# Optimization experiments

Hardware: AMD Instinct MI355X
Metric: run time of the kernel (lower is better)

## Reference

```python
import jax, jax.numpy as jnp
import numpy as np

NUM_NODES = 20000
NUM_EDGES = 65536
WIDTH = 64
EDGE_FEAT = 6
HIDDEN = 128


def setup_inputs() -> dict:
    key = jax.random.key(0)
    ks = jax.random.split(key, 6)
    x = jax.random.normal(ks[0], (NUM_NODES, WIDTH), dtype=jnp.float32)
    edge_attr = jax.random.normal(ks[1], (NUM_EDGES, EDGE_FEAT), dtype=jnp.float32)
    # weight-generating MLP params (the `nn` callable), fan-in scaled
    W1 = jax.random.normal(ks[2], (EDGE_FEAT, HIDDEN), dtype=jnp.float32) / np.sqrt(EDGE_FEAT)
    b1 = jnp.zeros((HIDDEN,), dtype=jnp.float32)
    W2 = jax.random.normal(ks[3], (HIDDEN, WIDTH * WIDTH), dtype=jnp.float32) / np.sqrt(HIDDEN)
    b2 = jnp.zeros((WIDTH * WIDTH,), dtype=jnp.float32)
    senders = jax.random.randint(ks[4], (NUM_EDGES,), 0, NUM_NODES)
    receivers = jax.random.randint(ks[5], (NUM_EDGES,), 0, NUM_NODES)
    return {"x": x, "edge_attr": edge_attr, "W1": W1, "b1": b1,
            "W2": W2, "b2": b2, "senders": senders, "receivers": receivers}


def reference(x, edge_attr, W1, b1, W2, b2, senders, receivers):
    n_segs, width = x.shape
    # nn(edge_attr): (E, width*width) edge-conditioned weights
    h = jax.nn.relu(edge_attr @ W1 + b1)
    weight = (h @ W2 + b2).reshape(-1, width, width)  # (E, w, w)
    # gather sender features, per-edge (1,w) @ (w,w) matmul -> (E, w)
    msgs = jnp.einsum('ew,ewv->ev', x[senders], weight)
    # scatter-sum messages into receiver nodes (aggr == 'sum')
    return jax.ops.segment_sum(msgs, receivers, num_segments=n_segs)
```

## Files before the change

### kernel.cpp

```cpp
#include <hip/hip_runtime.h>
#include <stdint.h>

typedef _Float16 f16;
typedef f16 f16x8 __attribute__((ext_vector_type(8)));
typedef float f32x4 __attribute__((ext_vector_type(4)));

#define NUM_NODES 20000
#define NUM_EDGES 65536
#define WIDTH 64
#define EDGE_FEAT 6
#define HIDDEN 128
#define BM 128
#define PADCH 132
#define XPAD 72

#define XH_HALFS (NUM_NODES * WIDTH)
#define XCONV_BLKS 625
#define W2G_HALFS (PADCH * 4096)
#define OUT_FLOATS (NUM_NODES * WIDTH)
#define ZBLKS 313

__device__ __forceinline__ void gload_lds16(const f16* g, f16* l) {
  __builtin_amdgcn_global_load_lds(
      (const __attribute__((address_space(1))) unsigned int*)g,
      (__attribute__((address_space(3))) unsigned int*)l, 16, 0, 0);
}

__global__ __launch_bounds__(256) void prep_kernel(
    const float* __restrict__ x, const float* __restrict__ W2,
    const float* __restrict__ b2, f16* __restrict__ ws_h,
    float* __restrict__ out)
{
  f16* x_h = ws_h;
  f16* W2g = ws_h + XH_HALFS;
  const int blk = blockIdx.x, tid = threadIdx.x;

  if (blk < PADCH) {
    const int ki = blk;
    if (ki > HIDDEN) {
      f16x8 z;
      #pragma unroll
      for (int u = 0; u < 8; ++u) z[u] = (f16)0.f;
      *(f16x8*)&W2g[(size_t)ki * 4096 + tid * 16] = z;
      *(f16x8*)&W2g[(size_t)ki * 4096 + tid * 16 + 8] = z;
      return;
    }
    __shared__ float row[4096];
    const float* srcrow;
    if (ki < HIDDEN) {
      const float4* src = (const float4*)(W2 + (size_t)ki * 4096);
      #pragma unroll
      for (int i = 0; i < 4; ++i) {
        float4 v = src[tid + 256 * i];
        *(float4*)&row[(tid + 256 * i) * 4] = v;
      }
      __syncthreads();
      srcrow = row;
    } else {
      srcrow = b2;
    }
    const int obase = tid * 16;
    f16x8 outv0, outv1;
    #pragma unroll
    for (int u = 0; u < 8; ++u) {
      int o = obase + u;
      int n = o >> 6, pg = (o >> 3) & 7, j = o & 7;
      int k = (pg ^ (n & 7)) * 8 + j;
      outv0[u] = (f16)srcrow[k * 64 + n];
    }
    #pragma unroll
    for (int u = 0; u < 8; ++u) {
      int o = obase + 8 + u;
      int n = o >> 6, pg = (o >> 3) & 7, j = o & 7;
      int k = (pg ^ (n & 7)) * 8 + j;
      outv1[u] = (f16)srcrow[k * 64 + n];
    }
    *(f16x8*)&W2g[(size_t)ki * 4096 + obase] = outv0;
    *(f16x8*)&W2g[(size_t)ki * 4096 + obase + 8] = outv1;
  } else if (blk < PADCH + XCONV_BLKS) {
    int idx = (blk - PADCH) * 2048 + tid * 8;
    if (idx + 8 <= XH_HALFS) {
      float4 a = *(const float4*)(x + idx);
      float4 b = *(const float4*)(x + idx + 4);
      f16x8 hv;
      hv[0] = (f16)a.x; hv[1] = (f16)a.y; hv[2] = (f16)a.z; hv[3] = (f16)a.w;
      hv[4] = (f16)b.x; hv[5] = (f16)b.y; hv[6] = (f16)b.z; hv[7] = (f16)b.w;
      *(f16x8*)&x_h[idx] = hv;
    }
  } else {
    int base = (blk - PADCH - XCONV_BLKS) * 4096 + tid * 16;
    float4 z = {0.f, 0.f, 0.f, 0.f};
    #pragma unroll
    for (int i = 0; i < 4; ++i) {
      int idx = base + i * 4;
      if (idx + 4 <= OUT_FLOATS) *(float4*)(out + idx) = z;
    }
  }
}

__global__ __launch_bounds__(256, 3) void nnconv_kernel(
    const float* __restrict__ ea, const float* __restrict__ W1,
    const float* __restrict__ b1, const int* __restrict__ senders,
    const int* __restrict__ receivers, const f16* __restrict__ ws_h,
    float* __restrict__ out)
{
  const f16* x_h = ws_h;
  const f16* W2g = ws_h + XH_HALFS;
  __shared__ __align__(16) f16 xt[BM][XPAD];
  __shared__ __align__(16) f16 Bring[2 * 8192];

  const int tid = threadIdx.x;
  const int lane = tid & 63, wid = tid >> 6;
  const int quad = lane >> 4, l15 = lane & 15;
  const int mhalf = wid >> 1, nhalf = wid & 1;
  const int e0 = blockIdx.x * BM;
  const int mbase = mhalf * 64;

#define STAGE(GIDX, GP)                                                       \
  {                                                                           \
    _Pragma("unroll") for (int i_ = 0; i_ < 4; ++i_) {                        \
      int slice_ = wid + 4 * i_;                                              \
      gload_lds16(W2g + (size_t)(GIDX) * 8192 + slice_ * 512 + (lane << 3),   \
                  &Bring[(GP) * 8192 + slice_ * 512]);                        \
    }                                                                         \
  }
  STAGE(0, 0);

  {
    int r = tid >> 1, half = tid & 1;
    int s = senders[e0 + r];
    const uint4* src = (const uint4*)(x_h + (size_t)s * WIDTH + half * 32);
    uint4* dst = (uint4*)&xt[r][half * 32];
    #pragma unroll
    for (int i = 0; i < 4; ++i) dst[i] = src[i];
  }

  float ear[4][6];
  #pragma unroll
  for (int t = 0; t < 4; ++t) {
    const float* p = ea + (size_t)(e0 + mbase + t * 16 + l15) * EDGE_FEAT;
    #pragma unroll
    for (int f = 0; f < 6; ++f) ear[t][f] = p[f];
  }

  int boff[2][2];
  #pragma unroll
  for (int kc = 0; kc < 2; ++kc)
    #pragma unroll
    for (int nt = 0; nt < 2; ++nt) {
      int n = (nhalf * 2 + nt) * 16 + l15;
      int g = kc * 4 + quad;
      boff[kc][nt] = n * 64 + (g ^ (n & 7)) * 8;
    }

#define HCOMP(KI, HV)                                                         \
  {                                                                           \
    float b1c_ = b1[(KI)];                                                    \
    float w1c_[6];                                                            \
    _Pragma("unroll") for (int f = 0; f < 6; ++f)                             \
      w1c_[f] = W1[f * HIDDEN + (KI)];                                        \
    _Pragma("unroll") for (int t = 0; t < 4; ++t) {                           \
      float s_ = b1c_;                                                        \
      _Pragma("unroll") for (int f = 0; f < 6; ++f)                           \
        s_ = fmaf(ear[t][f], w1c_[f], s_);                                    \
      HV[t] = (f16)fmaxf(s_, 0.f);                                            \
    }                                                                         \
  }

  f16 h0[4], h1[4];
  HCOMP(0, h0);
  HCOMP(1, h1);

  __syncthreads();

  f16x8 xf[4][2];
  #pragma unroll
  for (int t = 0; t < 4; ++t)
    #pragma unroll
    for (int kc = 0; kc < 2; ++kc)
      xf[t][kc] = *(const f16x8*)&xt[mbase + t * 16 + l15][kc * 32 + quad * 8];

  f32x4 acc[4][2];
  #pragma unroll
  for (int t = 0; t < 4; ++t)
    #pragma unroll
    for (int nt = 0; nt < 2; ++nt)
      acc[t][nt] = (f32x4){0.f, 0.f, 0.f, 0.f};

#define RD(DST, CBASE)                                                        \
  _Pragma("unroll") for (int kc = 0; kc < 2; ++kc)                            \
    _Pragma("unroll") for (int nt = 0; nt < 2; ++nt)                          \
      DST[kc][nt] = *(const f16x8*)&(CBASE)[boff[kc][nt]];

#define MM(BF, HV)                                                            \
  __builtin_amdgcn_s_setprio(1);                                              \
  _Pragma("unroll") for (int t = 0; t < 4; ++t) {                             \
    f16x8 sa0_ = xf[t][0] * HV[t];                                            \
    f16x8 sa1_ = xf[t][1] * HV[t];                                            \
    _Pragma("unroll") for (int nt = 0; nt < 2; ++nt) {                        \
      acc[t][nt] = __builtin_amdgcn_mfma_f32_16x16x32_f16(                    \
          sa0_, BF[0][nt], acc[t][nt], 0, 0, 0);                              \
      acc[t][nt] = __builtin_amdgcn_mfma_f32_16x16x32_f16(                    \
          sa1_, BF[1][nt], acc[t][nt], 0, 0, 0);                              \
    }                                                                         \
  }                                                                           \
  __builtin_amdgcn_s_setprio(0);

  #pragma unroll 1
  for (int g = 0; g < 64; ++g) {
    asm volatile("s_waitcnt vmcnt(0) lgkmcnt(0)\n\ts_barrier" ::: "memory");
    __builtin_amdgcn_sched_barrier(0);
    STAGE(g + 1, (g + 1) & 1);
    __builtin_amdgcn_sched_barrier(0);

    f16* gb = &Bring[(g & 1) * 8192];
    f16x8 bfP[2][2], bfQ[2][2];
    RD(bfP, gb);
    RD(bfQ, gb + 4096);

    int cn0 = 2 * g + 2; if (cn0 > 127) cn0 = 127;
    int cn1 = 2 * g + 3; if (cn1 > 127) cn1 = 127;

    MM(bfP, h0);
    HCOMP(cn0, h0);
    MM(bfQ, h1);
    HCOMP(cn1, h1);
  }

  asm volatile("s_waitcnt vmcnt(0) lgkmcnt(0)\n\ts_barrier" ::: "memory");
  __builtin_amdgcn_sched_barrier(0);
  {
    f16x8 bfP[2][2];
    RD(bfP, &Bring[0]);
    __builtin_amdgcn_s_setprio(1);
    #pragma unroll
    for (int t = 0; t < 4; ++t)
      #pragma unroll
      for (int nt = 0; nt < 2; ++nt) {
        acc[t][nt] = __builtin_amdgcn_mfma_f32_16x16x32_f16(
            xf[t][0], bfP[0][nt], acc[t][nt], 0, 0, 0);
        acc[t][nt] = __builtin_amdgcn_mfma_f32_16x16x32_f16(
            xf[t][1], bfP[1][nt], acc[t][nt], 0, 0, 0);
      }
    __builtin_amdgcn_s_setprio(0);
  }
#undef STAGE
#undef RD
#undef MM
#undef HCOMP

  #pragma unroll
  for (int t = 0; t < 4; ++t) {
    int ebase = e0 + mbase + t * 16 + quad * 4;
    int rc[4];
    #pragma unroll
    for (int r = 0; r < 4; ++r) rc[r] = receivers[ebase + r];
    #pragma unroll
    for (int nt = 0; nt < 2; ++nt) {
      int v = (nhalf * 2 + nt) * 16 + l15;
      #pragma unroll
      for (int r = 0; r < 4; ++r)
        atomicAdd(out + (size_t)rc[r] * WIDTH + v, acc[t][nt][r]);
    }
  }
}

extern "C" void kernel_launch(void* const* d_in, const int* in_sizes, int n_in,
                              void* d_out, int out_size, void* d_ws, size_t ws_size,
                              hipStream_t stream) {
  const float* x  = (const float*)d_in[0];
  const float* ea = (const float*)d_in[1];
  const float* W1 = (const float*)d_in[2];
  const float* b1 = (const float*)d_in[3];
  const float* W2 = (const float*)d_in[4];
  const float* b2 = (const float*)d_in[5];
  const int* snd  = (const int*)d_in[6];
  const int* rcv  = (const int*)d_in[7];
  float* out = (float*)d_out;
  f16* wsh = (f16*)d_ws;

  const int prep_grid = PADCH + XCONV_BLKS + ZBLKS;
  prep_kernel<<<prep_grid, 256, 0, stream>>>(x, W2, b2, wsh, out);
  nnconv_kernel<<<NUM_EDGES / BM, 256, 0, stream>>>(ea, W1, b1, snd, rcv, wsh, out);
}
```

Measured before the change: 165.2 us.

## Halve edge tile to 64 and stage one hidden channel per iteration

Cuts the edge tile per block from 128 to 64, so twice as many blocks are launched, and raises the occupancy hint to 4 blocks per SM. The W2 staging is restructured to one hidden channel (4096 halves) per iteration over 128 iterations instead of two channels over 64, which halves the LDS ring. The aim is more parallelism and occupancy. In exchange, every W2 byte is streamed from L2 by twice as many blocks, and each block pays twice as many barriers for less MFMA work.

```diff
diff --git a/kernel.cpp b/kernel.cpp
--- a/kernel.cpp
+++ b/kernel.cpp
@@ -10,7 +10,7 @@
 #define WIDTH 64
 #define EDGE_FEAT 6
 #define HIDDEN 128
-#define BM 128
+#define BM 64
 #define PADCH 132
 #define XPAD 72
 
@@ -98,7 +98,7 @@
   }
 }
 
-__global__ __launch_bounds__(256, 3) void nnconv_kernel(
+__global__ __launch_bounds__(256, 4) void nnconv_kernel(
     const float* __restrict__ ea, const float* __restrict__ W1,
     const float* __restrict__ b1, const int* __restrict__ senders,
     const int* __restrict__ receivers, const f16* __restrict__ ws_h,
@@ -107,37 +107,37 @@
   const f16* x_h = ws_h;
   const f16* W2g = ws_h + XH_HALFS;
   __shared__ __align__(16) f16 xt[BM][XPAD];
-  __shared__ __align__(16) f16 Bring[2 * 8192];
+  __shared__ __align__(16) f16 Bb[2][4096];
 
   const int tid = threadIdx.x;
   const int lane = tid & 63, wid = tid >> 6;
   const int quad = lane >> 4, l15 = lane & 15;
   const int mhalf = wid >> 1, nhalf = wid & 1;
   const int e0 = blockIdx.x * BM;
-  const int mbase = mhalf * 64;
-
-#define STAGE(GIDX, GP)                                                       \
+  const int mbase = mhalf * 32;
+
+#define STAGE(CI, SP)                                                         \
   {                                                                           \
-    _Pragma("unroll") for (int i_ = 0; i_ < 4; ++i_) {                        \
+    _Pragma("unroll") for (int i_ = 0; i_ < 2; ++i_) {                        \
       int slice_ = wid + 4 * i_;                                              \
-      gload_lds16(W2g + (size_t)(GIDX) * 8192 + slice_ * 512 + (lane << 3),   \
-                  &Bring[(GP) * 8192 + slice_ * 512]);                        \
+      gload_lds16(W2g + (size_t)(CI) * 4096 + slice_ * 512 + (lane << 3),     \
+                  &Bb[SP][slice_ * 512]);                                     \
     }                                                                         \
   }
   STAGE(0, 0);
 
   {
-    int r = tid >> 1, half = tid & 1;
+    int r = tid >> 2, q = tid & 3;
     int s = senders[e0 + r];
-    const uint4* src = (const uint4*)(x_h + (size_t)s * WIDTH + half * 32);
-    uint4* dst = (uint4*)&xt[r][half * 32];
-    #pragma unroll
-    for (int i = 0; i < 4; ++i) dst[i] = src[i];
-  }
-
-  float ear[4][6];
-  #pragma unroll
-  for (int t = 0; t < 4; ++t) {
+    const uint4* src = (const uint4*)(x_h + (size_t)s * WIDTH + q * 16);
+    uint4* dst = (uint4*)&xt[r][q * 16];
+    dst[0] = src[0];
+    dst[1] = src[1];
+  }
+
+  float ear[2][6];
+  #pragma unroll
+  for (int t = 0; t < 2; ++t) {
     const float* p = ea + (size_t)(e0 + mbase + t * 16 + l15) * EDGE_FEAT;
     #pragma unroll
     for (int f = 0; f < 6; ++f) ear[t][f] = p[f];
@@ -148,7 +148,7 @@
   for (int kc = 0; kc < 2; ++kc)
     #pragma unroll
     for (int nt = 0; nt < 2; ++nt) {
-      int n = (nhalf * 2 + nt) * 16 + l15;
+      int n = nhalf * 32 + nt * 16 + l15;
       int g = kc * 4 + quad;
       boff[kc][nt] = n * 64 + (g ^ (n & 7)) * 8;
     }
@@ -159,7 +159,7 @@
     float w1c_[6];                                                            \
     _Pragma("unroll") for (int f = 0; f < 6; ++f)                             \
       w1c_[f] = W1[f * HIDDEN + (KI)];                                        \
-    _Pragma("unroll") for (int t = 0; t < 4; ++t) {                           \
+    _Pragma("unroll") for (int t = 0; t < 2; ++t) {                           \
       float s_ = b1c_;                                                        \
       _Pragma("unroll") for (int f = 0; f < 6; ++f)                           \
         s_ = fmaf(ear[t][f], w1c_[f], s_);                                    \
@@ -167,97 +167,102 @@
     }                                                                         \
   }
 
-  f16 h0[4], h1[4];
-  HCOMP(0, h0);
-  HCOMP(1, h1);
+  f16 hnxt[2];
+  HCOMP(0, hnxt);
 
   __syncthreads();
 
-  f16x8 xf[4][2];
-  #pragma unroll
-  for (int t = 0; t < 4; ++t)
+  f16x8 xf[2][2];
+  #pragma unroll
+  for (int t = 0; t < 2; ++t)
     #pragma unroll
     for (int kc = 0; kc < 2; ++kc)
       xf[t][kc] = *(const f16x8*)&xt[mbase + t * 16 + l15][kc * 32 + quad * 8];
 
-  f32x4 acc[4][2];
-  #pragma unroll
-  for (int t = 0; t < 4; ++t)
+  f32x4 acc[2][2];
+  #pragma unroll
+  for (int t = 0; t < 2; ++t)
     #pragma unroll
     for (int nt = 0; nt < 2; ++nt)
       acc[t][nt] = (f32x4){0.f, 0.f, 0.f, 0.f};
 
-#define RD(DST, CBASE)                                                        \
-  _Pragma("unroll") for (int kc = 0; kc < 2; ++kc)                            \
-    _Pragma("unroll") for (int nt = 0; nt < 2; ++nt)                          \
-      DST[kc][nt] = *(const f16x8*)&(CBASE)[boff[kc][nt]];
-
-#define MM(BF, HV)                                                            \
-  __builtin_amdgcn_s_setprio(1);                                              \
-  _Pragma("unroll") for (int t = 0; t < 4; ++t) {                             \
-    f16x8 sa0_ = xf[t][0] * HV[t];                                            \
-    f16x8 sa1_ = xf[t][1] * HV[t];                                            \
-    _Pragma("unroll") for (int nt = 0; nt < 2; ++nt) {                        \
-      acc[t][nt] = __builtin_amdgcn_mfma_f32_16x16x32_f16(                    \
-          sa0_, BF[0][nt], acc[t][nt], 0, 0, 0);                              \
-      acc[t][nt] = __builtin_amdgcn_mfma_f32_16x16x32_f16(                    \
-          sa1_, BF[1][nt], acc[t][nt], 0, 0, 0);                              \
-    }                                                                         \
-  }                                                                           \
-  __builtin_amdgcn_s_setprio(0);
-
   #pragma unroll 1
-  for (int g = 0; g < 64; ++g) {
+  for (int k = 0; k < 128; ++k) {
     asm volatile("s_waitcnt vmcnt(0) lgkmcnt(0)\n\ts_barrier" ::: "memory");
     __builtin_amdgcn_sched_barrier(0);
-    STAGE(g + 1, (g + 1) & 1);
+    STAGE(k + 1, (k + 1) & 1);
     __builtin_amdgcn_sched_barrier(0);
 
-    f16* gb = &Bring[(g & 1) * 8192];
-    f16x8 bfP[2][2], bfQ[2][2];
-    RD(bfP, gb);
-    RD(bfQ, gb + 4096);
-
-    int cn0 = 2 * g + 2; if (cn0 > 127) cn0 = 127;
-    int cn1 = 2 * g + 3; if (cn1 > 127) cn1 = 127;
-
-    MM(bfP, h0);
-    HCOMP(cn0, h0);
-    MM(bfQ, h1);
-    HCOMP(cn1, h1);
+    f16 hv[2];
+    #pragma unroll
+    for (int t = 0; t < 2; ++t) hv[t] = hnxt[t];
+
+    const f16* gb = &Bb[k & 1][0];
+    f16x8 bf[2][2];
+    #pragma unroll
+    for (int kc = 0; kc < 2; ++kc)
+      #pragma unroll
+      for (int nt = 0; nt < 2; ++nt)
+        bf[kc][nt] = *(const f16x8*)&gb[boff[kc][nt]];
+
+    int kn = (k + 1 < 128) ? k + 1 : 127;
+    HCOMP(kn, hnxt);
+
+    f16x8 sa0[2], sa1[2];
+    #pragma unroll
+    for (int t = 0; t < 2; ++t) {
+      sa0[t] = xf[t][0] * hv[t];
+      sa1[t] = xf[t][1] * hv[t];
+    }
+    __builtin_amdgcn_s_setprio(1);
+    #pragma unroll
+    for (int t = 0; t < 2; ++t)
+      #pragma unroll
+      for (int nt = 0; nt < 2; ++nt)
+        acc[t][nt] = __builtin_amdgcn_mfma_f32_16x16x32_f16(
+            sa0[t], bf[0][nt], acc[t][nt], 0, 0, 0);
+    #pragma unroll
+    for (int t = 0; t < 2; ++t)
+      #pragma unroll
+      for (int nt = 0; nt < 2; ++nt)
+        acc[t][nt] = __builtin_amdgcn_mfma_f32_16x16x32_f16(
+            sa1[t], bf[1][nt], acc[t][nt], 0, 0, 0);
+    __builtin_amdgcn_s_setprio(0);
   }
 
   asm volatile("s_waitcnt vmcnt(0) lgkmcnt(0)\n\ts_barrier" ::: "memory");
   __builtin_amdgcn_sched_barrier(0);
   {
-    f16x8 bfP[2][2];
-    RD(bfP, &Bring[0]);
+    f16x8 bf[2][2];
+    #pragma unroll
+    for (int kc = 0; kc < 2; ++kc)
+      #pragma unroll
+      for (int nt = 0; nt < 2; ++nt)
+        bf[kc][nt] = *(const f16x8*)&Bb[0][boff[kc][nt]];
     __builtin_amdgcn_s_setprio(1);
     #pragma unroll
-    for (int t = 0; t < 4; ++t)
+    for (int t = 0; t < 2; ++t)
       #pragma unroll
       for (int nt = 0; nt < 2; ++nt) {
         acc[t][nt] = __builtin_amdgcn_mfma_f32_16x16x32_f16(
-            xf[t][0], bfP[0][nt], acc[t][nt], 0, 0, 0);
-        acc[t][nt] = __builtin_amdgcn_mfma_f32_16x16x32_f16(
-            xf[t][1], bfP[1][nt], acc[t][nt], 0, 0, 0);
+            xf[t][0], bf[0][nt], acc[t][nt], 0, 0, 0);
+        acc[t][nt] = __builtin_amdgcn_mfma_f32_16x16x32_f16(
+            xf[t][1], bf[1][nt], acc[t][nt], 0, 0, 0);
       }
     __builtin_amdgcn_s_setprio(0);
   }
 #undef STAGE
-#undef RD
-#undef MM
 #undef HCOMP
 
   #pragma unroll
-  for (int t = 0; t < 4; ++t) {
+  for (int t = 0; t < 2; ++t) {
     int ebase = e0 + mbase + t * 16 + quad * 4;
     int rc[4];
     #pragma unroll
     for (int r = 0; r < 4; ++r) rc[r] = receivers[ebase + r];
     #pragma unroll
     for (int nt = 0; nt < 2; ++nt) {
-      int v = (nhalf * 2 + nt) * 16 + l15;
+      int v = nhalf * 32 + nt * 16 + l15;
       #pragma unroll
       for (int r = 0; r < 4; ++r)
         atomicAdd(out + (size_t)rc[r] * WIDTH + v, acc[t][nt][r]);
```

New measurement: 160.6 us. -2.8%, faster.

## Precompute hidden activations into LDS and use a 3-slot single-chunk W2 ring

Applied to the files above, without the earlier changes.

The first MLP layer's activations for the whole edge tile are now computed once up front into a shared hbuf from edge features staged in LDS, instead of being interleaved per hidden unit inside the main loop. The W2 staging changes from a double-buffered two-chunk ring to a triple-buffered one-chunk ring with partial vmcnt waits, so loads stay in flight across barriers. The loop is unrolled six-fold, and the dead zero-padding chunks are dropped from prep. LDS use rises to about 75KB, so the launch bound drops from 3 to 2 blocks per CU, trading occupancy for a lighter main loop.

```diff
diff --git a/kernel.cpp b/kernel.cpp
--- a/kernel.cpp
+++ b/kernel.cpp
@@ -11,12 +11,13 @@
 #define EDGE_FEAT 6
 #define HIDDEN 128
 #define BM 128
-#define PADCH 132
+#define NCHUNK 129
 #define XPAD 72
+#define HPAD 130
 
 #define XH_HALFS (NUM_NODES * WIDTH)
 #define XCONV_BLKS 625
-#define W2G_HALFS (PADCH * 4096)
+#define W2G_HALFS (NCHUNK * 4096)
 #define OUT_FLOATS (NUM_NODES * WIDTH)
 #define ZBLKS 313
 
@@ -35,17 +36,9 @@
   f16* W2g = ws_h + XH_HALFS;
   const int blk = blockIdx.x, tid = threadIdx.x;
 
-  if (blk < PADCH) {
+  if (blk < NCHUNK) {
+    __shared__ float row[4096];
     const int ki = blk;
-    if (ki > HIDDEN) {
-      f16x8 z;
-      #pragma unroll
-      for (int u = 0; u < 8; ++u) z[u] = (f16)0.f;
-      *(f16x8*)&W2g[(size_t)ki * 4096 + tid * 16] = z;
-      *(f16x8*)&W2g[(size_t)ki * 4096 + tid * 16 + 8] = z;
-      return;
-    }
-    __shared__ float row[4096];
     const float* srcrow;
     if (ki < HIDDEN) {
       const float4* src = (const float4*)(W2 + (size_t)ki * 4096);
@@ -77,8 +70,8 @@
     }
     *(f16x8*)&W2g[(size_t)ki * 4096 + obase] = outv0;
     *(f16x8*)&W2g[(size_t)ki * 4096 + obase + 8] = outv1;
-  } else if (blk < PADCH + XCONV_BLKS) {
-    int idx = (blk - PADCH) * 2048 + tid * 8;
+  } else if (blk < NCHUNK + XCONV_BLKS) {
+    int idx = (blk - NCHUNK) * 2048 + tid * 8;
     if (idx + 8 <= XH_HALFS) {
       float4 a = *(const float4*)(x + idx);
       float4 b = *(const float4*)(x + idx + 4);
@@ -88,7 +81,7 @@
       *(f16x8*)&x_h[idx] = hv;
     }
   } else {
-    int base = (blk - PADCH - XCONV_BLKS) * 4096 + tid * 16;
+    int base = (blk - NCHUNK - XCONV_BLKS) * 4096 + tid * 16;
     float4 z = {0.f, 0.f, 0.f, 0.f};
     #pragma unroll
     for (int i = 0; i < 4; ++i) {
@@ -98,7 +91,7 @@
   }
 }
 
-__global__ __launch_bounds__(256, 3) void nnconv_kernel(
+__global__ __launch_bounds__(256, 2) void nnconv_kernel(
     const float* __restrict__ ea, const float* __restrict__ W1,
     const float* __restrict__ b1, const int* __restrict__ senders,
     const int* __restrict__ receivers, const f16* __restrict__ ws_h,
@@ -107,7 +100,8 @@
   const f16* x_h = ws_h;
   const f16* W2g = ws_h + XH_HALFS;
   __shared__ __align__(16) f16 xt[BM][XPAD];
-  __shared__ __align__(16) f16 Bring[2 * 8192];
+  __shared__ __align__(16) f16 hbuf[HIDDEN * HPAD];
+  __shared__ __align__(16) f16 ring[3 * 4096];
 
   const int tid = threadIdx.x;
   const int lane = tid & 63, wid = tid >> 6;
@@ -116,15 +110,17 @@
   const int e0 = blockIdx.x * BM;
   const int mbase = mhalf * 64;
 
-#define STAGE(GIDX, GP)                                                       \
-  {                                                                           \
-    _Pragma("unroll") for (int i_ = 0; i_ < 4; ++i_) {                        \
-      int slice_ = wid + 4 * i_;                                              \
-      gload_lds16(W2g + (size_t)(GIDX) * 8192 + slice_ * 512 + (lane << 3),   \
-                  &Bring[(GP) * 8192 + slice_ * 512]);                        \
-    }                                                                         \
-  }
-  STAGE(0, 0);
+  const f16* wsrc = W2g + wid * 1024 + (lane << 3);
+  const int stg_off = wid * 1024;
+
+  gload_lds16(wsrc, &ring[stg_off]);
+  gload_lds16(wsrc + 512, &ring[stg_off + 512]);
+  gload_lds16(wsrc + 4096, &ring[4096 + stg_off]);
+  gload_lds16(wsrc + 4096 + 512, &ring[4096 + stg_off + 512]);
+
+  float* eaf = (float*)&ring[2 * 4096];
+  if (tid < 192)
+    ((float4*)eaf)[tid] = ((const float4*)(ea + (size_t)e0 * EDGE_FEAT))[tid];
 
   {
     int r = tid >> 1, half = tid & 1;
@@ -135,50 +131,49 @@
     for (int i = 0; i < 4; ++i) dst[i] = src[i];
   }
 
-  float ear[4][6];
-  #pragma unroll
-  for (int t = 0; t < 4; ++t) {
-    const float* p = ea + (size_t)(e0 + mbase + t * 16 + l15) * EDGE_FEAT;
-    #pragma unroll
-    for (int f = 0; f < 6; ++f) ear[t][f] = p[f];
-  }
+  __syncthreads();
+
+  {
+    const int k = tid >> 1, half = tid & 1;
+    float b1c = b1[k];
+    float w1c[6];
+    #pragma unroll
+    for (int f = 0; f < 6; ++f) w1c[f] = W1[f * HIDDEN + k];
+    f16* hrow = &hbuf[k * HPAD + half * 64];
+    const float* er = eaf + half * 64 * EDGE_FEAT;
+    #pragma unroll 2
+    for (int g8 = 0; g8 < 8; ++g8) {
+      f16x8 hv;
+      #pragma unroll
+      for (int j = 0; j < 8; ++j) {
+        const float* p = er + (g8 * 8 + j) * EDGE_FEAT;
+        float s = b1c;
+        #pragma unroll
+        for (int f = 0; f < 6; ++f) s = fmaf(p[f], w1c[f], s);
+        hv[j] = (f16)fmaxf(s, 0.f);
+      }
+      *(f16x8*)&hrow[g8 * 8] = hv;
+    }
+  }
+
+  f16x8 xf[4][2];
+  #pragma unroll
+  for (int t = 0; t < 4; ++t)
+    #pragma unroll
+    for (int kc = 0; kc < 2; ++kc)
+      xf[t][kc] = *(const f16x8*)&xt[mbase + t * 16 + l15][kc * 32 + quad * 8];
 
   int boff[2][2];
   #pragma unroll
   for (int kc = 0; kc < 2; ++kc)
     #pragma unroll
     for (int nt = 0; nt < 2; ++nt) {
-      int n = (nhalf * 2 + nt) * 16 + l15;
+      int n = nhalf * 32 + nt * 16 + l15;
       int g = kc * 4 + quad;
       boff[kc][nt] = n * 64 + (g ^ (n & 7)) * 8;
     }
 
-#define HCOMP(KI, HV)                                                         \
-  {                                                                           \
-    float b1c_ = b1[(KI)];                                                    \
-    float w1c_[6];                                                            \
-    _Pragma("unroll") for (int f = 0; f < 6; ++f)                             \
-      w1c_[f] = W1[f * HIDDEN + (KI)];                                        \
-    _Pragma("unroll") for (int t = 0; t < 4; ++t) {                           \
-      float s_ = b1c_;                                                        \
-      _Pragma("unroll") for (int f = 0; f < 6; ++f)                           \
-        s_ = fmaf(ear[t][f], w1c_[f], s_);                                    \
-      HV[t] = (f16)fmaxf(s_, 0.f);                                            \
-    }                                                                         \
-  }
-
-  f16 h0[4], h1[4];
-  HCOMP(0, h0);
-  HCOMP(1, h1);
-
-  __syncthreads();
-
-  f16x8 xf[4][2];
-  #pragma unroll
-  for (int t = 0; t < 4; ++t)
-    #pragma unroll
-    for (int kc = 0; kc < 2; ++kc)
-      xf[t][kc] = *(const f16x8*)&xt[mbase + t * 16 + l15][kc * 32 + quad * 8];
+  const f16* hb = &hbuf[mbase + l15];
 
   f32x4 acc[4][2];
   #pragma unroll
@@ -187,67 +182,80 @@
     for (int nt = 0; nt < 2; ++nt)
       acc[t][nt] = (f32x4){0.f, 0.f, 0.f, 0.f};
 
-#define RD(DST, CBASE)                                                        \
-  _Pragma("unroll") for (int kc = 0; kc < 2; ++kc)                            \
-    _Pragma("unroll") for (int nt = 0; nt < 2; ++nt)                          \
-      DST[kc][nt] = *(const f16x8*)&(CBASE)[boff[kc][nt]];
-
-#define MM(BF, HV)                                                            \
-  __builtin_amdgcn_s_setprio(1);                                              \
-  _Pragma("unroll") for (int t = 0; t < 4; ++t) {                             \
-    f16x8 sa0_ = xf[t][0] * HV[t];                                            \
-    f16x8 sa1_ = xf[t][1] * HV[t];                                            \
-    _Pragma("unroll") for (int nt = 0; nt < 2; ++nt) {                        \
-      acc[t][nt] = __builtin_amdgcn_mfma_f32_16x16x32_f16(                    \
-          sa0_, BF[0][nt], acc[t][nt], 0, 0, 0);                              \
-      acc[t][nt] = __builtin_amdgcn_mfma_f32_16x16x32_f16(                    \
-          sa1_, BF[1][nt], acc[t][nt], 0, 0, 0);                              \
+  __syncthreads();
+
+#define STEP(K, SLOT, STG, SDST, VM)                                          \
+  {                                                                           \
+    asm volatile("s_waitcnt vmcnt(%0) lgkmcnt(0)\n\ts_barrier"                \
+                 :: "i"(VM) : "memory");                                      \
+    __builtin_amdgcn_sched_barrier(0);                                        \
+    if (STG) {                                                                \
+      const f16* s_ = wsrc + (size_t)((K) + 2) * 4096;                        \
+      f16* d_ = &ring[(SDST) * 4096 + stg_off];                               \
+      gload_lds16(s_, d_);                                                    \
+      gload_lds16(s_ + 512, d_ + 512);                                        \
     }                                                                         \
-  }                                                                           \
-  __builtin_amdgcn_s_setprio(0);
+    __builtin_amdgcn_sched_barrier(0);                                        \
+    f16 hv_[4];                                                               \
+    _Pragma("unroll") for (int t = 0; t < 4; ++t)                             \
+      hv_[t] = hb[(K) * HPAD + t * 16];                                       \
+    const f16* gb_ = &ring[(SLOT) * 4096];                                    \
+    f16x8 bf_[2][2];                                                          \
+    _Pragma("unroll") for (int kc = 0; kc < 2; ++kc)                          \
+      _Pragma("unroll") for (int nt = 0; nt < 2; ++nt)                        \
+        bf_[kc][nt] = *(const f16x8*)&gb_[boff[kc][nt]];                      \
+    f16x8 sa0_[4], sa1_[4];                                                   \
+    _Pragma("unroll") for (int t = 0; t < 4; ++t) {                           \
+      sa0_[t] = xf[t][0] * hv_[t];                                            \
+      sa1_[t] = xf[t][1] * hv_[t];                                            \
+    }                                                                         \
+    __builtin_amdgcn_s_setprio(1);                                            \
+    _Pragma("unroll") for (int t = 0; t < 4; ++t)                             \
+      _Pragma("unroll") for (int nt = 0; nt < 2; ++nt)                        \
+        acc[t][nt] = __builtin_amdgcn_mfma_f32_16x16x32_f16(                  \
+            sa0_[t], bf_[0][nt], acc[t][nt], 0, 0, 0);                        \
+    _Pragma("unroll") for (int t = 0; t < 4; ++t)                             \
+      _Pragma("unroll") for (int nt = 0; nt < 2; ++nt)                        \
+        acc[t][nt] = __builtin_amdgcn_mfma_f32_16x16x32_f16(                  \
+            sa1_[t], bf_[1][nt], acc[t][nt], 0, 0, 0);                        \
+    __builtin_amdgcn_s_setprio(0);                                            \
+  }
 
   #pragma unroll 1
-  for (int g = 0; g < 64; ++g) {
-    asm volatile("s_waitcnt vmcnt(0) lgkmcnt(0)\n\ts_barrier" ::: "memory");
-    __builtin_amdgcn_sched_barrier(0);
-    STAGE(g + 1, (g + 1) & 1);
-    __builtin_amdgcn_sched_barrier(0);
-
-    f16* gb = &Bring[(g & 1) * 8192];
-    f16x8 bfP[2][2], bfQ[2][2];
-    RD(bfP, gb);
-    RD(bfQ, gb + 4096);
-
-    int cn0 = 2 * g + 2; if (cn0 > 127) cn0 = 127;
-    int cn1 = 2 * g + 3; if (cn1 > 127) cn1 = 127;
-
-    MM(bfP, h0);
-    HCOMP(cn0, h0);
-    MM(bfQ, h1);
-    HCOMP(cn1, h1);
-  }
+  for (int kb = 0; kb < 126; kb += 6) {
+    STEP(kb + 0, 0, 1, 2, 2);
+    STEP(kb + 1, 1, 1, 0, 2);
+    STEP(kb + 2, 2, 1, 1, 2);
+    STEP(kb + 3, 0, 1, 2, 2);
+    STEP(kb + 4, 1, 1, 0, 2);
+    STEP(kb + 5, 2, 1, 1, 2);
+  }
+  STEP(126, 0, 1, 2, 2);
+  STEP(127, 1, 0, 0, 2);
 
   asm volatile("s_waitcnt vmcnt(0) lgkmcnt(0)\n\ts_barrier" ::: "memory");
   __builtin_amdgcn_sched_barrier(0);
   {
-    f16x8 bfP[2][2];
-    RD(bfP, &Bring[0]);
+    const f16* gb_ = &ring[2 * 4096];
+    f16x8 bf_[2][2];
+    #pragma unroll
+    for (int kc = 0; kc < 2; ++kc)
+      #pragma unroll
+      for (int nt = 0; nt < 2; ++nt)
+        bf_[kc][nt] = *(const f16x8*)&gb_[boff[kc][nt]];
     __builtin_amdgcn_s_setprio(1);
     #pragma unroll
     for (int t = 0; t < 4; ++t)
       #pragma unroll
       for (int nt = 0; nt < 2; ++nt) {
         acc[t][nt] = __builtin_amdgcn_mfma_f32_16x16x32_f16(
-            xf[t][0], bfP[0][nt], acc[t][nt], 0, 0, 0);
+            xf[t][0], bf_[0][nt], acc[t][nt], 0, 0, 0);
         acc[t][nt] = __builtin_amdgcn_mfma_f32_16x16x32_f16(
-            xf[t][1], bfP[1][nt], acc[t][nt], 0, 0, 0);
+            xf[t][1], bf_[1][nt], acc[t][nt], 0, 0, 0);
       }
     __builtin_amdgcn_s_setprio(0);
   }
-#undef STAGE
-#undef RD
-#undef MM
-#undef HCOMP
+#undef STEP
 
   #pragma unroll
   for (int t = 0; t < 4; ++t) {
@@ -279,7 +287,7 @@
   float* out = (float*)d_out;
   f16* wsh = (f16*)d_ws;
 
-  const int prep_grid = PADCH + XCONV_BLKS + ZBLKS;
+  const int prep_grid = NCHUNK + XCONV_BLKS + ZBLKS;
   prep_kernel<<<prep_grid, 256, 0, stream>>>(x, W2, b2, wsh, out);
   nnconv_kernel<<<NUM_EDGES / BM, 256, 0, stream>>>(ea, W1, b1, snd, rcv, wsh, out);
 }
```

Result: faster. 145.7 us (median of 2 runs) (-11.8%).
